# Kernel tuning notes

Measured on AMD Instinct MI355X. Metric: run time of the kernel, lower is better.

Reference implementation:

```python
import jax, jax.numpy as jnp
import numpy as np

C = 64      # in_channels
NX = 432    # pseudo-image x dim
NY = 496    # pseudo-image y dim
B = 4       # batch size
M_PER = 12000  # pillars per sample (KITTI PointPillars max)


def setup_inputs() -> dict:
    key = jax.random.key(0)
    rng = np.random.default_rng(0)
    feats = jax.random.normal(key, (B * M_PER, C), dtype=jnp.float32)
    # Build per-sample UNIQUE spatial indices (real voxelization never emits
    # duplicate pillar coords within a sample; duplicates would make the
    # scatter-set nondeterministic).
    coords = []
    for b in range(B):
        flat = rng.permutation(NX * NY)[:M_PER]
        x = flat // NY
        y = flat % NY
        z = np.zeros_like(x)
        coords.append(np.stack([z, y, x], axis=1))  # (M_PER, 3) in z,y,x order
    batch_indices = jnp.asarray(np.concatenate(coords, axis=0), dtype=jnp.int32)
    sample_indices = jnp.asarray(np.repeat(np.arange(B), M_PER), dtype=jnp.int32)
    return {
        "batch_pillar_features": feats,
        "batch_indices": batch_indices,
        "sample_indices": sample_indices,
        "batch_size": B,
    }


def reference(batch_pillar_features, batch_indices, sample_indices, batch_size):
    # Single fused scatter over the whole batch: flatten (sample, x, y) into
    # one linear index into a (B*NX*NY, C) canvas, then reshape.
    spatial = batch_indices[:, 2].astype(jnp.int32) * NY + batch_indices[:, 1].astype(jnp.int32)
    flat = sample_indices.astype(jnp.int32) * (NX * NY) + spatial  # (M,)
    canvas = jnp.zeros((batch_size * NX * NY, C), dtype=batch_pillar_features.dtype)
    canvas = canvas.at[flat].set(batch_pillar_features)            # scatter rows
    canvas = canvas.reshape(batch_size, NX, NY, C).transpose(0, 3, 1, 2)  # (B,C,NX,NY)
    return jnp.flip(canvas, axis=2)  # torch.flip(dims=[2])
```

## Files before the change

### kernel.cpp

```cpp
#include <hip/hip_runtime.h>

#define C_CH 64
#define NX 432
#define NY 496
#define NYQ 124
#define PLANEQ (NX * NYQ)


__global__ void scatter_idx_kernel(const int* __restrict__ bidx,
                                   const int* __restrict__ sidx,
                                   int* __restrict__ map, int M) {
    int m = blockIdx.x * blockDim.x + threadIdx.x;
    if (m >= M) return;
    int y = bidx[3 * m + 1];
    int x = bidx[3 * m + 2];
    int s = sidx[m];
    map[(size_t)s * (NX * NY) + (size_t)(NX - 1 - x) * NY + y] = m;
}

__global__ void gather_out_kernel(const float4* __restrict__ feats4,
                                  const int4* __restrict__ map,
                                  float4* __restrict__ out, int nsq) {
    int i = blockIdx.x * blockDim.x + threadIdx.x;
    if (i >= nsq) return;
    const int h = blockIdx.y;
    int b  = i / PLANEQ;
    int sq = i - b * PLANEQ;
    int4 mm = map[i];

    float4* ob = out + ((size_t)b * C_CH + (size_t)h * 16) * PLANEQ + sq;
    const float4* fbase = feats4 + (size_t)h * 4;

    #pragma unroll
    for (int cg = 0; cg < 4; ++cg) {
        float4 f0 = make_float4(0.f, 0.f, 0.f, 0.f);
        float4 f1 = f0, f2 = f0, f3 = f0;
        if (mm.x >= 0) f0 = fbase[(size_t)mm.x * 16 + cg];
        if (mm.y >= 0) f1 = fbase[(size_t)mm.y * 16 + cg];
        if (mm.z >= 0) f2 = fbase[(size_t)mm.z * 16 + cg];
        if (mm.w >= 0) f3 = fbase[(size_t)mm.w * 16 + cg];
        float4* p = ob + (size_t)(cg * 4) * PLANEQ;
        p[0]          = make_float4(f0.x, f1.x, f2.x, f3.x);
        p[PLANEQ]     = make_float4(f0.y, f1.y, f2.y, f3.y);
        p[2 * PLANEQ] = make_float4(f0.z, f1.z, f2.z, f3.z);
        p[3 * PLANEQ] = make_float4(f0.w, f1.w, f2.w, f3.w);
    }
}


__global__ void zero_out_kernel(float4* __restrict__ out, int nq) {
    int i = blockIdx.x * blockDim.x + threadIdx.x;
    if (i < nq) out[i] = make_float4(0.f, 0.f, 0.f, 0.f);
}

__global__ void scatter_feats_kernel(const float* __restrict__ feats,
                                     const int* __restrict__ bidx,
                                     const int* __restrict__ sidx,
                                     float* __restrict__ out, int M) {
    int tid = blockIdx.x * blockDim.x + threadIdx.x;
    if (tid >= M * C_CH) return;
    int m = tid >> 6;
    int c = tid & (C_CH - 1);
    int y = bidx[3 * m + 1];
    int x = bidx[3 * m + 2];
    int s = sidx[m];
    size_t o = (((size_t)s * C_CH + c) * NX + (NX - 1 - x)) * NY + y;
    out[o] = feats[tid];
}

extern "C" void kernel_launch(void* const* d_in, const int* in_sizes, int n_in,
                              void* d_out, int out_size, void* d_ws, size_t ws_size,
                              hipStream_t stream) {
    const float* feats = (const float*)d_in[0];
    const int*   bidx  = (const int*)d_in[1];
    const int*   sidx  = (const int*)d_in[2];
    float*       out   = (float*)d_out;

    const int M = in_sizes[0] / C_CH;
    const int B = out_size / (C_CH * NX * NY);

    const size_t map_elems = (size_t)B * NX * NY;
    const size_t map_bytes = map_elems * sizeof(int);

    if (ws_size >= map_bytes) {
        int* map = (int*)d_ws;
        hipMemsetAsync(map, 0xFF, map_bytes, stream);
        scatter_idx_kernel<<<(M + 255) / 256, 256, 0, stream>>>(bidx, sidx, map, M);
        {
            int nsq = B * PLANEQ;
            dim3 grid((nsq + 255) / 256, 4);
            gather_out_kernel<<<grid, 256, 0, stream>>>(
                (const float4*)feats, (const int4*)map, (float4*)out, nsq);
        }
    } else {
        int nq = out_size / 4;
        zero_out_kernel<<<(nq + 255) / 256, 256, 0, stream>>>((float4*)out, nq);
        int nt = M * C_CH;
        scatter_feats_kernel<<<(nt + 255) / 256, 256, 0, stream>>>(
            feats, bidx, sidx, out, M);
    }
}
```

Baseline: 53.82 us.

## Replace channel-group gather with per-plane block writing contiguous output planes

The gather kernel is restructured so that each block owns one (batch, channel) output plane and loops over it, reading the index map and fetching a single scalar feature per pillar. This gives fully contiguous streaming writes per plane and a simpler address pattern, instead of each thread writing 16 strided planes. The cost is re-reading the index map once per channel, scattered 4-byte feature loads, and a coarse grid of only B*64 large blocks that may underfill the GPU.

```diff
diff --git a/kernel.cpp b/kernel.cpp
--- a/kernel.cpp
+++ b/kernel.cpp
@@ -18,32 +18,25 @@
     map[(size_t)s * (NX * NY) + (size_t)(NX - 1 - x) * NY + y] = m;
 }
 
-__global__ void gather_out_kernel(const float4* __restrict__ feats4,
-                                  const int4* __restrict__ map,
-                                  float4* __restrict__ out, int nsq) {
-    int i = blockIdx.x * blockDim.x + threadIdx.x;
-    if (i >= nsq) return;
-    const int h = blockIdx.y;
-    int b  = i / PLANEQ;
-    int sq = i - b * PLANEQ;
-    int4 mm = map[i];
+__global__ __launch_bounds__(1024) void plane_write_kernel(
+        const float* __restrict__ feats,
+        const int4* __restrict__ map4,
+        float4* __restrict__ out) {
+    const int plane = blockIdx.x;
+    const int b = plane >> 6;
+    const int c = plane & (C_CH - 1);
 
-    float4* ob = out + ((size_t)b * C_CH + (size_t)h * 16) * PLANEQ + sq;
-    const float4* fbase = feats4 + (size_t)h * 4;
+    const int4* mp = map4 + (size_t)b * PLANEQ;
+    float4* ob = out + (size_t)plane * PLANEQ;
 
-    #pragma unroll
-    for (int cg = 0; cg < 4; ++cg) {
-        float4 f0 = make_float4(0.f, 0.f, 0.f, 0.f);
-        float4 f1 = f0, f2 = f0, f3 = f0;
-        if (mm.x >= 0) f0 = fbase[(size_t)mm.x * 16 + cg];
-        if (mm.y >= 0) f1 = fbase[(size_t)mm.y * 16 + cg];
-        if (mm.z >= 0) f2 = fbase[(size_t)mm.z * 16 + cg];
-        if (mm.w >= 0) f3 = fbase[(size_t)mm.w * 16 + cg];
-        float4* p = ob + (size_t)(cg * 4) * PLANEQ;
-        p[0]          = make_float4(f0.x, f1.x, f2.x, f3.x);
-        p[PLANEQ]     = make_float4(f0.y, f1.y, f2.y, f3.y);
-        p[2 * PLANEQ] = make_float4(f0.z, f1.z, f2.z, f3.z);
-        p[3 * PLANEQ] = make_float4(f0.w, f1.w, f2.w, f3.w);
+    for (int q = threadIdx.x; q < PLANEQ; q += 1024) {
+        int4 mm = mp[q];
+        float4 v = make_float4(0.f, 0.f, 0.f, 0.f);
+        if (mm.x >= 0) v.x = feats[(size_t)mm.x * C_CH + c];
+        if (mm.y >= 0) v.y = feats[(size_t)mm.y * C_CH + c];
+        if (mm.z >= 0) v.z = feats[(size_t)mm.z * C_CH + c];
+        if (mm.w >= 0) v.w = feats[(size_t)mm.w * C_CH + c];
+        ob[q] = v;
     }
 }
 
@@ -86,12 +79,8 @@
         int* map = (int*)d_ws;
         hipMemsetAsync(map, 0xFF, map_bytes, stream);
         scatter_idx_kernel<<<(M + 255) / 256, 256, 0, stream>>>(bidx, sidx, map, M);
-        {
-            int nsq = B * PLANEQ;
-            dim3 grid((nsq + 255) / 256, 4);
-            gather_out_kernel<<<grid, 256, 0, stream>>>(
-                (const float4*)feats, (const int4*)map, (float4*)out, nsq);
-        }
+        plane_write_kernel<<<B * C_CH, 1024, 0, stream>>>(
+            feats, (const int4*)map, (float4*)out);
     } else {
         int nq = out_size / 4;
         zero_out_kernel<<<(nq + 255) / 256, 256, 0, stream>>>((float4*)out, nq);
```

After: 62.17 us. 1.16x slower.
